# Performance work log

Measured on AMD Instinct MI355X. Metric: run time of the kernel, lower is better.

## Reference

```python
import jax, jax.numpy as jnp
import numpy as np

RATIO = 0.2
MIX_ALPHA = 0.5
TEMPERATURE = 0.1
EPS = 1e-12  # F.normalize eps


def setup_inputs() -> dict:
    key = jax.random.key(0)
    z = jax.random.normal(key, (16384, 256), dtype=jnp.float32)
    return {"z": z}


def reference(z):
    B = z.shape[0]
    n_hard = max(1, int(B * RATIO))

    # L2-normalize rows (F.normalize with eps clamp)
    norm = jnp.maximum(jnp.linalg.norm(z, axis=-1, keepdims=True), EPS)
    z_norm = z / norm

    # [B, B] cosine similarity, diagonal excluded
    sim = z_norm @ z_norm.T
    diag = jnp.eye(B, dtype=bool)
    sim = jnp.where(diag, -jnp.inf, sim)
    logits = sim / TEMPERATURE  # softmax(logits) == sim_probs

    # Batched sampling: replaces the per-sample Python loop with one fused pass
    key = jax.random.key(42)
    k_src, k_tgt, k_alpha = jax.random.split(key, 3)
    src_idx = jax.random.randint(k_src, (n_hard,), 0, B)  # torch.randint
    # categorical over logits rows == multinomial over softmax probs
    tgt_idx = jax.random.categorical(k_tgt, logits[src_idx], axis=-1)
    alpha = jax.random.uniform(k_alpha, (n_hard, 1), dtype=z.dtype) * MIX_ALPHA

    hard_negs = alpha * z[src_idx] + (1.0 - alpha) * z[tgt_idx]  # [n_hard, D]
    return hard_negs
```

## Files before the change

### kernel.cpp

```cpp
#include <hip/hip_runtime.h>
#include <stdint.h>
#include <math.h>

#define BN 16384
#define DK 256
#define NH 3276
#define MPAD 3328
#define NJB 26
#define NCB 128

typedef __attribute__((ext_vector_type(8))) short short8;
typedef __attribute__((ext_vector_type(4))) float f32x4;

__host__ __device__ __forceinline__ void tf2x32(uint32_t k0, uint32_t k1,
                                                uint32_t c0, uint32_t c1,
                                                uint32_t& o0, uint32_t& o1) {
  uint32_t ks2 = 0x1BD11BDAu ^ k0 ^ k1;
  uint32_t x0 = c0 + k0, x1 = c1 + k1;
#define RR(d) { x0 += x1; x1 = (x1 << d) | (x1 >> (32 - d)); x1 ^= x0; }
  RR(13) RR(15) RR(26) RR(6)   x0 += k1;  x1 += ks2 + 1u;
  RR(17) RR(29) RR(16) RR(24)  x0 += ks2; x1 += k0  + 2u;
  RR(13) RR(15) RR(26) RR(6)   x0 += k0;  x1 += k1  + 3u;
  RR(17) RR(29) RR(16) RR(24)  x0 += k1;  x1 += ks2 + 4u;
  RR(13) RR(15) RR(26) RR(6)   x0 += ks2; x1 += k0  + 5u;
#undef RR
  o0 = x0; o1 = x1;
}

__device__ __forceinline__ uint32_t rand32_at(uint32_t k0, uint32_t k1, uint32_t p) {
  uint32_t x0, x1; tf2x32(k0, k1, 0u, p, x0, x1);
  return x0 ^ x1;
}

__device__ __forceinline__ float unif01_from_bits(uint32_t bits) {
  return __uint_as_float((bits >> 9) | 0x3f800000u) - 1.0f;
}

__device__ __forceinline__ float gumbel_at(uint32_t k0, uint32_t k1, uint32_t p) {
  uint32_t bits = rand32_at(k0, k1, p);
  float f = unif01_from_bits(bits);
  float u = fmaxf(f, 1.17549435e-38f);
  float t = __log2f(u) * (-0.69314718055994531f);
  return __log2f(t) * (-0.69314718055994531f);
}

__device__ __forceinline__ unsigned long long packvc(float v, uint32_t c) {
  uint32_t u = __float_as_uint(v);
  u ^= ((int32_t)u < 0) ? 0xFFFFFFFFu : 0x80000000u;
  return ((unsigned long long)u << 32) | (unsigned long long)(~c);
}

__device__ __forceinline__ void split8(float4 a, float4 b, short8& h, short8& l) {
  float f[8] = {a.x, a.y, a.z, a.w, b.x, b.y, b.z, b.w};
#pragma unroll
  for (int i = 0; i < 8; ++i) {
    uint32_t u = __float_as_uint(f[i]);
    h[i] = (short)(u >> 16);
    float r = f[i] - __uint_as_float(u & 0xFFFF0000u);
    l[i] = (short)(__float_as_uint(r) >> 16);
  }
}

__global__ __launch_bounds__(256) void k_norm(const float* __restrict__ z,
                                              float* __restrict__ inv_norm) {
  int row  = blockIdx.x * 4 + (threadIdx.x >> 6);
  int lane = threadIdx.x & 63;
  float4 v = *(const float4*)&z[row * DK + lane * 4];
  float ss = v.x * v.x + v.y * v.y + v.z * v.z + v.w * v.w;
#pragma unroll
  for (int off = 32; off; off >>= 1) ss += __shfl_xor(ss, off, 64);
  if (lane == 0) inv_norm[row] = 1.0f / fmaxf(sqrtf(ss), 1e-12f);
}

__global__ __launch_bounds__(256) void k_setup(int* __restrict__ src_idx,
                                               unsigned long long* __restrict__ best,
                                               uint32_t k20, uint32_t k21) {
  int i = blockIdx.x * 256 + threadIdx.x;
  if (i < NH) {
    uint32_t bits = rand32_at(k20, k21, (uint32_t)i);
    src_idx[i] = (int)(bits & (uint32_t)(BN - 1));
    best[i] = 0ull;
  }
}

__global__ __launch_bounds__(256, 2) void k_main(const float* __restrict__ z,
                                                 const float* __restrict__ inv_norm,
                                                 const int* __restrict__ src_idx,
                                                 unsigned long long* __restrict__ best,
                                                 uint32_t kt0, uint32_t kt1) {
  __shared__ __align__(16) short As_hi[128 * 64];
  __shared__ __align__(16) short As_lo[128 * 64];
  __shared__ __align__(16) short Bs_hi[128 * 64];
  __shared__ __align__(16) short Bs_lo[128 * 64];

  const int flat = blockIdx.x;
  const int xcd = flat & 7, slot = flat >> 3;
  const int c_base = (xcd * 16 + (slot & 15)) * 128;
  const int j_base = (slot >> 4) * 128;

  const int t = threadIdx.x;
  const int lane = t & 63, w = t >> 6;
  const int g = t & 7;
  const int srow = t >> 3;

  int arow[4];
#pragma unroll
  for (int u = 0; u < 4; ++u)
    arow[u] = src_idx[min(j_base + srow + 32 * u, NH - 1)];

  f32x4 acc[4][4];
#pragma unroll
  for (int mt = 0; mt < 4; ++mt)
#pragma unroll
    for (int nt = 0; nt < 4; ++nt) acc[mt][nt] = (f32x4){0.f, 0.f, 0.f, 0.f};

  for (int kc = 0; kc < 4; ++kc) {
    const int k0 = kc * 64;
#pragma unroll
    for (int u = 0; u < 4; ++u) {
      int row = srow + 32 * u;
      int off = row * 64 + ((g ^ (row & 7)) * 8);
      const float* pa = z + (size_t)arow[u] * DK + k0 + g * 8;
      float4 a0 = *(const float4*)pa;
      float4 a1 = *(const float4*)(pa + 4);
      short8 h, l;
      split8(a0, a1, h, l);
      *(short8*)&As_hi[off] = h;
      *(short8*)&As_lo[off] = l;
      const float* pb = z + (size_t)(c_base + row) * DK + k0 + g * 8;
      float4 b0 = *(const float4*)pb;
      float4 b1 = *(const float4*)(pb + 4);
      split8(b0, b1, h, l);
      *(short8*)&Bs_hi[off] = h;
      *(short8*)&Bs_lo[off] = l;
    }
    __syncthreads();

    const int cl = lane & 15, q = lane >> 4;
    const int mrow0 = (w >> 1) * 64 + cl;
    const int nrow0 = (w & 1) * 64 + cl;
#pragma unroll
    for (int s = 0; s < 2; ++s) {
      short8 ah[4], al[4], bh[4], bl[4];
#pragma unroll
      for (int mt = 0; mt < 4; ++mt) {
        int row = mrow0 + mt * 16;
        int off = row * 64 + (((s * 4 + q) ^ (row & 7)) * 8);
        ah[mt] = *(const short8*)&As_hi[off];
        al[mt] = *(const short8*)&As_lo[off];
      }
#pragma unroll
      for (int nt = 0; nt < 4; ++nt) {
        int row = nrow0 + nt * 16;
        int off = row * 64 + (((s * 4 + q) ^ (row & 7)) * 8);
        bh[nt] = *(const short8*)&Bs_hi[off];
        bl[nt] = *(const short8*)&Bs_lo[off];
      }
#pragma unroll
      for (int mt = 0; mt < 4; ++mt)
#pragma unroll
        for (int nt = 0; nt < 4; ++nt) {
          acc[mt][nt] = __builtin_amdgcn_mfma_f32_16x16x32_bf16(ah[mt], bh[nt], acc[mt][nt], 0, 0, 0);
          acc[mt][nt] = __builtin_amdgcn_mfma_f32_16x16x32_bf16(ah[mt], bl[nt], acc[mt][nt], 0, 0, 0);
          acc[mt][nt] = __builtin_amdgcn_mfma_f32_16x16x32_bf16(al[mt], bh[nt], acc[mt][nt], 0, 0, 0);
        }
    }
    __syncthreads();
  }

  const int cl = lane & 15;
  const int q4 = (lane >> 4) * 4;
  const int coff = c_base + (w & 1) * 64;
  const int roff = j_base + (w >> 1) * 64;
  float invc[4]; int colg[4];
#pragma unroll
  for (int nt = 0; nt < 4; ++nt) {
    colg[nt] = coff + nt * 16 + cl;
    invc[nt] = inv_norm[colg[nt]];
  }
#pragma unroll
  for (int mt = 0; mt < 4; ++mt)
#pragma unroll
    for (int r = 0; r < 4; ++r) {
      int gj = roff + mt * 16 + q4 + r;
      int s = src_idx[min(gj, NH - 1)];
      float invs = inv_norm[s];
      uint32_t pbase = (uint32_t)gj * (uint32_t)BN;
      float bv = -INFINITY; uint32_t bc = 0;
#pragma unroll
      for (int nt = 0; nt < 4; ++nt) {
        float sim = acc[mt][nt][r] * invs * invc[nt];
        float gmb = gumbel_at(kt0, kt1, pbase + (uint32_t)colg[nt]);
        float tot = fmaf(sim, 10.0f, gmb);
        if (colg[nt] == s) tot = -INFINITY;
        if (tot > bv) { bv = tot; bc = (uint32_t)colg[nt]; }
      }
      unsigned long long key = packvc(bv, bc);
#pragma unroll
      for (int off = 1; off <= 8; off <<= 1) {
        unsigned long long o = __shfl_xor(key, off, 64);
        if (o > key) key = o;
      }
      if (cl == 0 && gj < NH) atomicMax(&best[gj], key);
    }
}

__global__ __launch_bounds__(64) void k_out(const float* __restrict__ z,
                                            const int* __restrict__ src_idx,
                                            const unsigned long long* __restrict__ best,
                                            float* __restrict__ out,
                                            uint32_t ka0, uint32_t ka1) {
  int j = blockIdx.x;
  int lane = threadIdx.x;
  int s = src_idx[j];
  int tgt = (int)(~((uint32_t)(best[j] & 0xFFFFFFFFull)));
  uint32_t bits = rand32_at(ka0, ka1, (uint32_t)j);
  float alpha = unif01_from_bits(bits) * 0.5f;
  float om = 1.0f - alpha;
  float4 a = *(const float4*)&z[s * DK + lane * 4];
  float4 b = *(const float4*)&z[tgt * DK + lane * 4];
  float4 o;
  o.x = alpha * a.x + om * b.x;
  o.y = alpha * a.y + om * b.y;
  o.z = alpha * a.z + om * b.z;
  o.w = alpha * a.w + om * b.w;
  *(float4*)&out[j * DK + lane * 4] = o;
}

extern "C" void kernel_launch(void* const* d_in, const int* in_sizes, int n_in,
                              void* d_out, int out_size, void* d_ws, size_t ws_size,
                              hipStream_t stream) {
  const float* z = (const float*)d_in[0];
  float* out = (float*)d_out;
  char* ws = (char*)d_ws;
  float*              inv_norm = (float*)(ws);
  int*                src_idx  = (int*)(ws + 65536);
  unsigned long long* best     = (unsigned long long*)(ws + 78656);

  uint32_t r0 = 0u, r1 = 42u;
  uint32_t ks0, ks1, kt0, kt1, ka0, ka1, k20, k21;
  tf2x32(r0, r1, 0u, 0u, ks0, ks1);
  tf2x32(r0, r1, 0u, 1u, kt0, kt1);
  tf2x32(r0, r1, 0u, 2u, ka0, ka1);
  tf2x32(ks0, ks1, 0u, 1u, k20, k21);

  k_norm <<<dim3(BN / 4), dim3(256), 0, stream>>>(z, inv_norm);
  k_setup<<<dim3((NH + 255) / 256), dim3(256), 0, stream>>>(src_idx, best, k20, k21);
  k_main <<<dim3(NCB * NJB), dim3(256), 0, stream>>>(z, inv_norm, src_idx, best, kt0, kt1);
  k_out  <<<dim3(NH), dim3(64), 0, stream>>>(z, src_idx, best, out, ka0, ka1);
}
```

Baseline: 304.8 us.

## Precompute bf16 hi/lo split once and stream tiles via global_load_lds

Adds a prep kernel that computes row norms and splits z into bf16 hi/lo arrays once, merging the norm and setup kernels into it. The main GEMM kernel then loads the pre-split tiles directly into LDS with global_load_lds, using a smaller 32-wide K chunk with a new swizzle and raising the occupancy hint to 4 blocks per CU. This removes the per-tile fp32 loads and repeated split arithmetic in the hot loop and halves LDS use, at the cost of an extra pass writing 16 MB of bf16 data and twice as many barriers per tile.

```diff
diff --git a/kernel.cpp b/kernel.cpp
--- a/kernel.cpp
+++ b/kernel.cpp
@@ -5,11 +5,11 @@
 #define BN 16384
 #define DK 256
 #define NH 3276
-#define MPAD 3328
 #define NJB 26
 #define NCB 128
 
 typedef __attribute__((ext_vector_type(8))) short short8;
+typedef __attribute__((ext_vector_type(4))) short short4v;
 typedef __attribute__((ext_vector_type(4))) float f32x4;
 
 __host__ __device__ __forceinline__ void tf2x32(uint32_t k0, uint32_t k1,
@@ -50,48 +50,58 @@
   return ((unsigned long long)u << 32) | (unsigned long long)(~c);
 }
 
-__device__ __forceinline__ void split8(float4 a, float4 b, short8& h, short8& l) {
-  float f[8] = {a.x, a.y, a.z, a.w, b.x, b.y, b.z, b.w};
-#pragma unroll
-  for (int i = 0; i < 8; ++i) {
-    uint32_t u = __float_as_uint(f[i]);
-    h[i] = (short)(u >> 16);
-    float r = f[i] - __uint_as_float(u & 0xFFFF0000u);
-    l[i] = (short)(__float_as_uint(r) >> 16);
+__device__ __forceinline__ void glds16(const unsigned short* g, short* l) {
+  __builtin_amdgcn_global_load_lds(
+      (const __attribute__((address_space(1))) void*)g,
+      (__attribute__((address_space(3))) void*)l, 16, 0, 0);
+}
+
+__global__ __launch_bounds__(256) void k_prep(const float* __restrict__ z,
+                                              float* __restrict__ inv_norm,
+                                              unsigned short* __restrict__ zh,
+                                              unsigned short* __restrict__ zl,
+                                              int* __restrict__ src_idx,
+                                              unsigned long long* __restrict__ best,
+                                              uint32_t k20, uint32_t k21) {
+  int b = blockIdx.x, t = threadIdx.x;
+  if (b < BN / 4) {
+    int row = b * 4 + (t >> 6), lane = t & 63;
+    float4 v = *(const float4*)&z[row * DK + lane * 4];
+    float ss = v.x * v.x + v.y * v.y + v.z * v.z + v.w * v.w;
+#pragma unroll
+    for (int off = 32; off; off >>= 1) ss += __shfl_xor(ss, off, 64);
+    if (lane == 0) inv_norm[row] = 1.0f / fmaxf(sqrtf(ss), 1e-12f);
+    float f[4] = {v.x, v.y, v.z, v.w};
+    short4v h, l;
+#pragma unroll
+    for (int i = 0; i < 4; ++i) {
+      uint32_t u = __float_as_uint(f[i]);
+      h[i] = (short)(u >> 16);
+      float r = f[i] - __uint_as_float(u & 0xFFFF0000u);
+      l[i] = (short)(__float_as_uint(r) >> 16);
+    }
+    *(short4v*)&zh[row * DK + lane * 4] = h;
+    *(short4v*)&zl[row * DK + lane * 4] = l;
+  } else {
+    int i = (b - BN / 4) * 256 + t;
+    if (i < NH) {
+      uint32_t bits = rand32_at(k20, k21, (uint32_t)i);
+      src_idx[i] = (int)(bits & (uint32_t)(BN - 1));
+      best[i] = 0ull;
+    }
   }
 }
 
-__global__ __launch_bounds__(256) void k_norm(const float* __restrict__ z,
-                                              float* __restrict__ inv_norm) {
-  int row  = blockIdx.x * 4 + (threadIdx.x >> 6);
-  int lane = threadIdx.x & 63;
-  float4 v = *(const float4*)&z[row * DK + lane * 4];
-  float ss = v.x * v.x + v.y * v.y + v.z * v.z + v.w * v.w;
-#pragma unroll
-  for (int off = 32; off; off >>= 1) ss += __shfl_xor(ss, off, 64);
-  if (lane == 0) inv_norm[row] = 1.0f / fmaxf(sqrtf(ss), 1e-12f);
-}
-
-__global__ __launch_bounds__(256) void k_setup(int* __restrict__ src_idx,
-                                               unsigned long long* __restrict__ best,
-                                               uint32_t k20, uint32_t k21) {
-  int i = blockIdx.x * 256 + threadIdx.x;
-  if (i < NH) {
-    uint32_t bits = rand32_at(k20, k21, (uint32_t)i);
-    src_idx[i] = (int)(bits & (uint32_t)(BN - 1));
-    best[i] = 0ull;
-  }
-}
-
-__global__ __launch_bounds__(256, 2) void k_main(const float* __restrict__ z,
+__global__ __launch_bounds__(256, 4) void k_main(const unsigned short* __restrict__ zh,
+                                                 const unsigned short* __restrict__ zl,
                                                  const float* __restrict__ inv_norm,
                                                  const int* __restrict__ src_idx,
                                                  unsigned long long* __restrict__ best,
                                                  uint32_t kt0, uint32_t kt1) {
-  __shared__ __align__(16) short As_hi[128 * 64];
-  __shared__ __align__(16) short As_lo[128 * 64];
-  __shared__ __align__(16) short Bs_hi[128 * 64];
-  __shared__ __align__(16) short Bs_lo[128 * 64];
+  __shared__ __align__(16) short As_hi[128 * 32];
+  __shared__ __align__(16) short As_lo[128 * 32];
+  __shared__ __align__(16) short Bs_hi[128 * 32];
+  __shared__ __align__(16) short Bs_lo[128 * 32];
 
   const int flat = blockIdx.x;
   const int xcd = flat & 7, slot = flat >> 3;
@@ -100,13 +110,25 @@
 
   const int t = threadIdx.x;
   const int lane = t & 63, w = t >> 6;
-  const int g = t & 7;
-  const int srow = t >> 3;
-
-  int arow[4];
-#pragma unroll
-  for (int u = 0; u < 4; ++u)
-    arow[u] = src_idx[min(j_base + srow + 32 * u, NH - 1)];
+
+  const int r0 = w * 32 + (lane >> 2);
+  const int r1 = r0 + 16;
+  const int u0 = (lane & 3) ^ ((r0 >> 1) & 3);
+  const int u1 = (lane & 3) ^ ((r1 >> 1) & 3);
+  const int ga0 = src_idx[min(j_base + r0, NH - 1)];
+  const int ga1 = src_idx[min(j_base + r1, NH - 1)];
+  const size_t offA0 = (size_t)ga0 * DK + u0 * 8;
+  const size_t offA1 = (size_t)ga1 * DK + u1 * 8;
+  const size_t offB0 = (size_t)(c_base + r0) * DK + u0 * 8;
+  const size_t offB1 = (size_t)(c_base + r1) * DK + u1 * 8;
+  short* dA = &As_hi[w * 1024];
+  short* dAl = &As_lo[w * 1024];
+  short* dB = &Bs_hi[w * 1024];
+  short* dBl = &Bs_lo[w * 1024];
+
+  const int cl = lane & 15, q = lane >> 4;
+  const int mb = (w >> 1) * 64 + cl;
+  const int nb = (w & 1) * 64 + cl;
 
   f32x4 acc[4][4];
 #pragma unroll
@@ -114,61 +136,43 @@
 #pragma unroll
     for (int nt = 0; nt < 4; ++nt) acc[mt][nt] = (f32x4){0.f, 0.f, 0.f, 0.f};
 
-  for (int kc = 0; kc < 4; ++kc) {
-    const int k0 = kc * 64;
-#pragma unroll
-    for (int u = 0; u < 4; ++u) {
-      int row = srow + 32 * u;
-      int off = row * 64 + ((g ^ (row & 7)) * 8);
-      const float* pa = z + (size_t)arow[u] * DK + k0 + g * 8;
-      float4 a0 = *(const float4*)pa;
-      float4 a1 = *(const float4*)(pa + 4);
-      short8 h, l;
-      split8(a0, a1, h, l);
-      *(short8*)&As_hi[off] = h;
-      *(short8*)&As_lo[off] = l;
-      const float* pb = z + (size_t)(c_base + row) * DK + k0 + g * 8;
-      float4 b0 = *(const float4*)pb;
-      float4 b1 = *(const float4*)(pb + 4);
-      split8(b0, b1, h, l);
-      *(short8*)&Bs_hi[off] = h;
-      *(short8*)&Bs_lo[off] = l;
-    }
+#pragma unroll
+  for (int kc = 0; kc < 8; ++kc) {
+    const int ko = kc * 32;
+    glds16(zh + offA0 + ko, dA);
+    glds16(zh + offA1 + ko, dA + 512);
+    glds16(zl + offA0 + ko, dAl);
+    glds16(zl + offA1 + ko, dAl + 512);
+    glds16(zh + offB0 + ko, dB);
+    glds16(zh + offB1 + ko, dB + 512);
+    glds16(zl + offB0 + ko, dBl);
+    glds16(zl + offB1 + ko, dBl + 512);
     __syncthreads();
 
-    const int cl = lane & 15, q = lane >> 4;
-    const int mrow0 = (w >> 1) * 64 + cl;
-    const int nrow0 = (w & 1) * 64 + cl;
-#pragma unroll
-    for (int s = 0; s < 2; ++s) {
-      short8 ah[4], al[4], bh[4], bl[4];
-#pragma unroll
-      for (int mt = 0; mt < 4; ++mt) {
-        int row = mrow0 + mt * 16;
-        int off = row * 64 + (((s * 4 + q) ^ (row & 7)) * 8);
-        ah[mt] = *(const short8*)&As_hi[off];
-        al[mt] = *(const short8*)&As_lo[off];
+    short8 bh[4], bl[4];
+#pragma unroll
+    for (int nt = 0; nt < 4; ++nt) {
+      int row = nb + nt * 16;
+      int off = row * 32 + (q ^ ((row >> 1) & 3)) * 8;
+      bh[nt] = *(const short8*)&Bs_hi[off];
+      bl[nt] = *(const short8*)&Bs_lo[off];
+    }
+#pragma unroll
+    for (int mt = 0; mt < 4; ++mt) {
+      int row = mb + mt * 16;
+      int off = row * 32 + (q ^ ((row >> 1) & 3)) * 8;
+      short8 ah = *(const short8*)&As_hi[off];
+      short8 al = *(const short8*)&As_lo[off];
+#pragma unroll
+      for (int nt = 0; nt < 4; ++nt) {
+        acc[mt][nt] = __builtin_amdgcn_mfma_f32_16x16x32_bf16(ah, bh[nt], acc[mt][nt], 0, 0, 0);
+        acc[mt][nt] = __builtin_amdgcn_mfma_f32_16x16x32_bf16(ah, bl[nt], acc[mt][nt], 0, 0, 0);
+        acc[mt][nt] = __builtin_amdgcn_mfma_f32_16x16x32_bf16(al, bh[nt], acc[mt][nt], 0, 0, 0);
       }
-#pragma unroll
-      for (int nt = 0; nt < 4; ++nt) {
-        int row = nrow0 + nt * 16;
-        int off = row * 64 + (((s * 4 + q) ^ (row & 7)) * 8);
-        bh[nt] = *(const short8*)&Bs_hi[off];
-        bl[nt] = *(const short8*)&Bs_lo[off];
-      }
-#pragma unroll
-      for (int mt = 0; mt < 4; ++mt)
-#pragma unroll
-        for (int nt = 0; nt < 4; ++nt) {
-          acc[mt][nt] = __builtin_amdgcn_mfma_f32_16x16x32_bf16(ah[mt], bh[nt], acc[mt][nt], 0, 0, 0);
-          acc[mt][nt] = __builtin_amdgcn_mfma_f32_16x16x32_bf16(ah[mt], bl[nt], acc[mt][nt], 0, 0, 0);
-          acc[mt][nt] = __builtin_amdgcn_mfma_f32_16x16x32_bf16(al[mt], bh[nt], acc[mt][nt], 0, 0, 0);
-        }
     }
     __syncthreads();
   }
 
-  const int cl = lane & 15;
   const int q4 = (lane >> 4) * 4;
   const int coff = c_base + (w & 1) * 64;
   const int roff = j_base + (w >> 1) * 64;
@@ -235,7 +239,9 @@
   char* ws = (char*)d_ws;
   float*              inv_norm = (float*)(ws);
   int*                src_idx  = (int*)(ws + 65536);
-  unsigned long long* best     = (unsigned long long*)(ws + 78656);
+  unsigned long long* best     = (unsigned long long*)(ws + 81920);
+  unsigned short*     zh       = (unsigned short*)(ws + 131072);
+  unsigned short*     zl       = (unsigned short*)(ws + 131072 + (size_t)BN * DK * 2);
 
   uint32_t r0 = 0u, r1 = 42u;
   uint32_t ks0, ks1, kt0, kt1, ka0, ka1, k20, k21;
@@ -244,8 +250,8 @@
   tf2x32(r0, r1, 0u, 2u, ka0, ka1);
   tf2x32(ks0, ks1, 0u, 1u, k20, k21);
 
-  k_norm <<<dim3(BN / 4), dim3(256), 0, stream>>>(z, inv_norm);
-  k_setup<<<dim3((NH + 255) / 256), dim3(256), 0, stream>>>(src_idx, best, k20, k21);
-  k_main <<<dim3(NCB * NJB), dim3(256), 0, stream>>>(z, inv_norm, src_idx, best, kt0, kt1);
-  k_out  <<<dim3(NH), dim3(64), 0, stream>>>(z, src_idx, best, out, ka0, ka1);
-}
+  k_prep<<<dim3(BN / 4 + (NH + 255) / 256), dim3(256), 0, stream>>>(
+      z, inv_norm, zh, zl, src_idx, best, k20, k21);
+  k_main<<<dim3(NCB * NJB), dim3(256), 0, stream>>>(zh, zl, inv_norm, src_idx, best, kt0, kt1);
+  k_out <<<dim3(NH), dim3(64), 0, stream>>>(z, src_idx, best, out, ka0, ka1);
+}
```

Measured after the change: 284.0 us. -6.8%, faster.
